# Kernel optimization log

Hardware: AMD Instinct MI355X
Metric: run time of the kernel (lower is better)

## Reference

```python
import jax, jax.numpy as jnp
import numpy as np
import math

B, S, D = 4, 2048, 1024
H, DK, DV = 16, 64, 64
EPS = 1e-5
SCALE = math.sqrt(1.0 / D)  # NOTE: original scales by 1/sqrt(d_model), not 1/sqrt(d_k)


def setup_inputs() -> dict:
    key = jax.random.key(0)
    ks = jax.random.split(key, 12)
    s = 0.02
    return {
        "Q": jax.random.normal(ks[0], (B, S, D), jnp.float32),
        "K": jax.random.normal(ks[1], (B, S, D), jnp.float32),
        "V": jax.random.normal(ks[2], (B, S, D), jnp.float32),
        # stacked per-head projection weights (torch Linear: y = x @ W.T + b)
        "Wq": jax.random.normal(ks[3], (H, D, DK), jnp.float32) * s,
        "bq": jnp.zeros((H, DK), jnp.float32),
        "Wk": jax.random.normal(ks[4], (H, D, DK), jnp.float32) * s,
        "bk": jnp.zeros((H, DK), jnp.float32),
        "Wv": jax.random.normal(ks[5], (H, D, DV), jnp.float32) * s,
        "bv": jnp.zeros((H, DV), jnp.float32),
        "Wo": jax.random.normal(ks[6], (H * DV, D), jnp.float32) * s,
        "bo": jnp.zeros((D,), jnp.float32),
        "gamma": jnp.ones((D,), jnp.float32),
        "beta": jnp.zeros((D,), jnp.float32),
    }


def reference(Q, K, V, Wq, bq, Wk, bk, Wv, bv, Wo, bo, gamma, beta):
    residual = Q
    # batched per-head projections: [B,S,D] x [H,D,dk] -> [B,H,S,dk]
    q = jnp.einsum("bsd,hdk->bhsk", Q, Wq) + bq[None, :, None, :]
    k = jnp.einsum("bsd,hdk->bhsk", K, Wk) + bk[None, :, None, :]
    v = jnp.einsum("bsd,hdv->bhsv", V, Wv) + bv[None, :, None, :]
    # scaled dot-product attention (scale uses d_model, per original code)
    attn = jax.nn.softmax(jnp.einsum("bhsk,bhtk->bhst", q, k) * SCALE, axis=-1)
    out = jnp.einsum("bhst,bhtv->bhsv", attn, v)  # [B,H,S,DV]
    # concat heads along feature dim: [B,S,H*DV]
    out = out.transpose(0, 2, 1, 3).reshape(B, S, H * DV)
    out = out @ Wo + bo  # output projection
    # dropout is identity in eval mode
    out = out + residual
    # BatchNorm1d over (B,S) per channel (training-mode batch stats)
    mean = jnp.mean(out, axis=(0, 1))
    var = jnp.mean(jnp.square(out - mean), axis=(0, 1))
    out = (out - mean) * jax.lax.rsqrt(var + EPS) * gamma + beta
    return out.transpose(0, 2, 1)  # (B, d_model, S)
```

## Files before the change

### kernel.cpp

```cpp
#include <hip/hip_runtime.h>

#define B_ 4
#define S_ 2048
#define D_ 1024
#define H_ 16
#define SCALE_ 0.03125f
#define EPS_ 1e-5f
#define NBS_ 8192

typedef unsigned short ushort_t;
typedef __attribute__((ext_vector_type(8))) short short8;
typedef __attribute__((ext_vector_type(4))) short short4v;
typedef __attribute__((ext_vector_type(4))) float floatx4;
typedef __attribute__((ext_vector_type(2))) unsigned int uint2v;

__device__ __forceinline__ ushort_t f2bf(float f) {
  union { float f; unsigned u; } v; v.f = f;
  unsigned r = v.u + 0x7fffu + ((v.u >> 16) & 1u);
  return (ushort_t)(r >> 16);
}

__device__ __forceinline__ float fast_exp2(float x) {
#if __has_builtin(__builtin_amdgcn_exp2f)
  return __builtin_amdgcn_exp2f(x);
#else
  return __expf(x * 0.6931471805599453f);
#endif
}

__device__ __forceinline__ short8 cvt8(float4 a, float4 b) {
  short8 r;
  r[0] = (short)f2bf(a.x); r[1] = (short)f2bf(a.y);
  r[2] = (short)f2bf(a.z); r[3] = (short)f2bf(a.w);
  r[4] = (short)f2bf(b.x); r[5] = (short)f2bf(b.y);
  r[6] = (short)f2bf(b.z); r[7] = (short)f2bf(b.w);
  return r;
}

__device__ __forceinline__ void gload16(const void* g, void* l) {
  __builtin_amdgcn_global_load_lds(
      (const __attribute__((address_space(1))) unsigned int*)g,
      (__attribute__((address_space(3))) unsigned int*)l, 16, 0, 0);
}

__global__ __launch_bounds__(256) void cvtx_k(const float* __restrict__ src,
                                              ushort_t* __restrict__ dst)
{
  size_t i = ((size_t)blockIdx.x * 256 + threadIdx.x) * 8;
  float4 a = *(const float4*)(src + i);
  float4 b = *(const float4*)(src + i + 4);
  *(short8*)(dst + i) = cvt8(a, b);
}

__global__ __launch_bounds__(256) void wtr_k(const float* __restrict__ src,
                                             ushort_t* __restrict__ dst, int mode)
{
  __shared__ float t[64][65];
  const int tr = blockIdx.x, tc = blockIdx.y;
  const float* sb; int sld;
  if (mode == 0) { sb = src + (size_t)tr * 65536 + (size_t)tc * 64 * 64; sld = 64; }
  else           { sb = src + (size_t)tc * 64 * 1024 + (size_t)tr * 64;  sld = 1024; }
  const int tid = threadIdx.x;
  const int rr = tid >> 2, cs = (tid & 3) * 16;
  const float* p = sb + (size_t)rr * sld + cs;
#pragma unroll
  for (int j = 0; j < 16; ++j) t[rr][cs + j] = p[j];
  __syncthreads();
  ushort_t* dp = dst + (size_t)(tr * 64 + rr) * 1024 + tc * 64 + cs;
#pragma unroll
  for (int j = 0; j < 16; ++j) dp[j] = f2bf(t[cs + j][rr]);
}

__global__ __launch_bounds__(256) void gemm_proj(
    const ushort_t* __restrict__ A, const ushort_t* __restrict__ Bw,
    const float* __restrict__ bias, ushort_t* __restrict__ outp, float scale)
{
  __shared__ ushort_t As[128 * 32];
  __shared__ ushort_t Bs[128 * 32];
  const int tid = threadIdx.x;
  const int wv = tid >> 6, lane = tid & 63, quad = lane >> 4, l16 = lane & 15;
  const int m0 = blockIdx.x * 128, n0 = blockIdx.y * 128;
  const int wm = wv & 1, wn = wv >> 1;
  const int lrow = lane >> 2, lkc = (lane & 3) * 8;

  floatx4 acc[4][4];
#pragma unroll
  for (int i = 0; i < 4; ++i)
#pragma unroll
    for (int j = 0; j < 4; ++j) acc[i][j] = (floatx4){0.f, 0.f, 0.f, 0.f};

  for (int k0 = 0; k0 < 1024; k0 += 32) {
    __syncthreads();
#pragma unroll
    for (int j = 0; j < 2; ++j) {
      const int rb = wv * 32 + j * 16;
      gload16(A + (size_t)(m0 + rb + lrow) * 1024 + k0 + lkc, (char*)As + rb * 64);
      gload16(Bw + (size_t)(n0 + rb + lrow) * 1024 + k0 + lkc, (char*)Bs + rb * 64);
    }
    __syncthreads();
    short8 af[4], bf[4];
#pragma unroll
    for (int i = 0; i < 4; ++i)
      af[i] = *(const short8*)&As[(wm * 64 + i * 16 + l16) * 32 + quad * 8];
#pragma unroll
    for (int i = 0; i < 4; ++i)
      bf[i] = *(const short8*)&Bs[(wn * 64 + i * 16 + l16) * 32 + quad * 8];
#pragma unroll
    for (int mi = 0; mi < 4; ++mi)
#pragma unroll
      for (int ni = 0; ni < 4; ++ni)
        acc[mi][ni] = __builtin_amdgcn_mfma_f32_16x16x32_bf16(
            af[mi], bf[ni], acc[mi][ni], 0, 0, 0);
  }

  const int b = m0 >> 11;
  const int sbase = (m0 & 2047) + wm * 64;
#pragma unroll
  for (int ni = 0; ni < 4; ++ni) {
    const int c = n0 + wn * 64 + ni * 16 + l16;
    const int h = c >> 6, nn = c & 63;
    const float bs = bias[c];
    ushort_t* op = outp + (size_t)(b * 16 + h) * 2048 * 64 + nn;
#pragma unroll
    for (int mi = 0; mi < 4; ++mi)
#pragma unroll
      for (int r = 0; r < 4; ++r) {
        int s = sbase + mi * 16 + quad * 4 + r;
        op[(size_t)s * 64] = f2bf((acc[mi][ni][r] + bs) * scale);
      }
  }
}

__global__ __launch_bounds__(256) void gemm_projT(
    const ushort_t* __restrict__ A, const ushort_t* __restrict__ Bw,
    const float* __restrict__ bias, ushort_t* __restrict__ outp)
{
  __shared__ ushort_t As[128 * 32];
  __shared__ ushort_t Bs[128 * 32];
  const int tid = threadIdx.x;
  const int wv = tid >> 6, lane = tid & 63, quad = lane >> 4, l16 = lane & 15;
  const int m0 = blockIdx.x * 128, n0 = blockIdx.y * 128;
  const int wm = wv & 1, wn = wv >> 1;
  const int lrow = lane >> 2, lkc = (lane & 3) * 8;

  floatx4 acc[4][4];
#pragma unroll
  for (int i = 0; i < 4; ++i)
#pragma unroll
    for (int j = 0; j < 4; ++j) acc[i][j] = (floatx4){0.f, 0.f, 0.f, 0.f};

  for (int k0 = 0; k0 < 1024; k0 += 32) {
    __syncthreads();
#pragma unroll
    for (int j = 0; j < 2; ++j) {
      const int rb = wv * 32 + j * 16;
      gload16(A + (size_t)(m0 + rb + lrow) * 1024 + k0 + lkc, (char*)As + rb * 64);
      gload16(Bw + (size_t)(n0 + rb + lrow) * 1024 + k0 + lkc, (char*)Bs + rb * 64);
    }
    __syncthreads();
    short8 af[4], bf[4];
#pragma unroll
    for (int i = 0; i < 4; ++i)
      af[i] = *(const short8*)&As[(wm * 64 + i * 16 + l16) * 32 + quad * 8];
#pragma unroll
    for (int i = 0; i < 4; ++i)
      bf[i] = *(const short8*)&Bs[(wn * 64 + i * 16 + l16) * 32 + quad * 8];
#pragma unroll
    for (int mi = 0; mi < 4; ++mi)
#pragma unroll
      for (int ni = 0; ni < 4; ++ni)
        acc[mi][ni] = __builtin_amdgcn_mfma_f32_16x16x32_bf16(
            af[mi], bf[ni], acc[mi][ni], 0, 0, 0);
  }

  const int b = m0 >> 11;
  const int sbase = (m0 & 2047) + wm * 64;
#pragma unroll
  for (int ni = 0; ni < 4; ++ni) {
    const int c = n0 + wn * 64 + ni * 16 + l16;
    const int h = c >> 6, nn = c & 63;
    const float bs = bias[c];
    ushort_t* op = outp + ((size_t)(b * 16 + h) * 64 + nn) * 2048;
#pragma unroll
    for (int mi = 0; mi < 4; ++mi) {
      int s0v = sbase + mi * 16 + quad * 4;
      short4v p;
#pragma unroll
      for (int r = 0; r < 4; ++r) p[r] = (short)f2bf(acc[mi][ni][r] + bs);
      *(short4v*)(op + s0v) = p;
    }
  }
}

__global__ __launch_bounds__(256) void gemm_oproj(
    const ushort_t* __restrict__ A, const ushort_t* __restrict__ Bw,
    const float* __restrict__ bo, const float* __restrict__ resid,
    float* __restrict__ y)
{
  __shared__ ushort_t As[128 * 32];
  __shared__ ushort_t Bs[128 * 32];
  const int tid = threadIdx.x;
  const int wv = tid >> 6, lane = tid & 63, quad = lane >> 4, l16 = lane & 15;
  const int m0 = blockIdx.x * 128, n0 = blockIdx.y * 128;
  const int wm = wv & 1, wn = wv >> 1;
  const int lrow = lane >> 2, lkc = (lane & 3) * 8;

  floatx4 acc[4][4];
#pragma unroll
  for (int i = 0; i < 4; ++i)
#pragma unroll
    for (int j = 0; j < 4; ++j) acc[i][j] = (floatx4){0.f, 0.f, 0.f, 0.f};

  for (int k0 = 0; k0 < 1024; k0 += 32) {
    __syncthreads();
#pragma unroll
    for (int j = 0; j < 2; ++j) {
      const int rb = wv * 32 + j * 16;
      gload16(A + (size_t)(m0 + rb + lrow) * 1024 + k0 + lkc, (char*)As + rb * 64);
      gload16(Bw + (size_t)(n0 + rb + lrow) * 1024 + k0 + lkc, (char*)Bs + rb * 64);
    }
    __syncthreads();
    short8 af[4], bf[4];
#pragma unroll
    for (int i = 0; i < 4; ++i)
      af[i] = *(const short8*)&As[(wm * 64 + i * 16 + l16) * 32 + quad * 8];
#pragma unroll
    for (int i = 0; i < 4; ++i)
      bf[i] = *(const short8*)&Bs[(wn * 64 + i * 16 + l16) * 32 + quad * 8];
#pragma unroll
    for (int mi = 0; mi < 4; ++mi)
#pragma unroll
      for (int ni = 0; ni < 4; ++ni)
        acc[mi][ni] = __builtin_amdgcn_mfma_f32_16x16x32_bf16(
            af[mi], bf[ni], acc[mi][ni], 0, 0, 0);
  }

  const int mb = m0 + wm * 64;
#pragma unroll
  for (int ni = 0; ni < 4; ++ni) {
    const int d = n0 + wn * 64 + ni * 16 + l16;
    const float bs = bo[d];
#pragma unroll
    for (int mi = 0; mi < 4; ++mi)
#pragma unroll
      for (int r = 0; r < 4; ++r) {
        int m = mb + mi * 16 + quad * 4 + r;
        y[(size_t)m * 1024 + d] = acc[mi][ni][r] + bs + resid[(size_t)m * 1024 + d];
      }
  }
}

__global__ __launch_bounds__(256, 3) void attn_k(
    const ushort_t* __restrict__ q, const ushort_t* __restrict__ k,
    const ushort_t* __restrict__ vt, ushort_t* __restrict__ ao)
{
  __shared__ ushort_t lds[24576];
  char* ldsb = (char*)lds;
  const int tid = threadIdx.x;
  const int wv = tid >> 6, lane = tid & 63, quad = lane >> 4, l16 = lane & 15;
  const int q0 = blockIdx.x * 128, h = blockIdx.y, b = blockIdx.z;
  const size_t bh = (size_t)(b * H_ + h) * S_;
  const ushort_t* vb = vt + (size_t)(b * H_ + h) * 64 * S_;

  short8 aq[2][2];
#pragma unroll
  for (int rb = 0; rb < 2; ++rb) {
    const ushort_t* qrow = q + (bh + q0 + wv * 32 + rb * 16 + l16) * 64;
    aq[rb][0] = *(const short8*)(qrow + quad * 8);
    aq[rb][1] = *(const short8*)(qrow + 32 + quad * 8);
  }

  floatx4 o[2][4];
  float ll[2] = {0.f, 0.f};
#pragma unroll
  for (int rb = 0; rb < 2; ++rb)
#pragma unroll
    for (int cb = 0; cb < 4; ++cb) o[rb][cb] = (floatx4){0.f, 0.f, 0.f, 0.f};

  const int swz = (l16 & 7) << 4;
  const int q8 = quad * 8;
  const int pb = 32768 + wv * 4096 + l16 * 128;

  auto stage = [&](int nb, int t0) {
#pragma unroll
    for (int i = 0; i < 4; ++i) {
      const int idx = wv * 4 + i;
      const int cb = (idx >> 1) & 3, hf = idx & 1;
      if (idx < 8)
        gload16(k + (bh + t0 + cb * 16 + l16) * 64 + hf * 32 + quad * 8,
                (char*)lds + nb * 8192 + idx * 1024);
      else
        gload16(vb + (size_t)(cb * 16 + l16) * S_ + t0 + hf * 32 + quad * 8,
                (char*)lds + 16384 + nb * 8192 + (idx - 8) * 1024);
    }
  };

  stage(0, 0);
  asm volatile("s_waitcnt vmcnt(0)" ::: "memory");
  __syncthreads();

  for (int t0 = 0; t0 < S_; t0 += 64) {
    const int nb = (t0 >> 6) & 1;
    const ushort_t* KsC = lds + nb * 4096;
    const ushort_t* VsC = lds + 8192 + nb * 4096;
    if (t0 + 64 < S_) stage(nb ^ 1, t0 + 64);

    floatx4 sc[2][4];
#pragma unroll
    for (int rb = 0; rb < 2; ++rb)
#pragma unroll
      for (int cb = 0; cb < 4; ++cb) sc[rb][cb] = (floatx4){0.f, 0.f, 0.f, 0.f};
    __builtin_amdgcn_s_setprio(1);
#pragma unroll
    for (int hf = 0; hf < 2; ++hf) {
      short8 bk[4];
#pragma unroll
      for (int cb = 0; cb < 4; ++cb)
        bk[cb] = *(const short8*)&KsC[(cb * 2 + hf) * 512 + lane * 8];
#pragma unroll
      for (int rb = 0; rb < 2; ++rb)
#pragma unroll
        for (int cb = 0; cb < 4; ++cb)
          sc[rb][cb] = __builtin_amdgcn_mfma_f32_16x16x32_bf16(
              bk[cb], aq[rb][hf], sc[rb][cb], 0, 0, 0);
    }
    __builtin_amdgcn_s_setprio(0);

    short8 bvf[2][4];
#pragma unroll
    for (int hf = 0; hf < 2; ++hf)
#pragma unroll
      for (int cb = 0; cb < 4; ++cb)
        bvf[hf][cb] = *(const short8*)&VsC[(cb * 2 + hf) * 512 + lane * 8];

#pragma unroll
    for (int rb = 0; rb < 2; ++rb) {
#pragma unroll
      for (int cb = 0; cb < 4; ++cb) {
        float p0 = fast_exp2(sc[rb][cb][0]);
        float p1 = fast_exp2(sc[rb][cb][1]);
        float p2 = fast_exp2(sc[rb][cb][2]);
        float p3 = fast_exp2(sc[rb][cb][3]);
        ll[rb] += (p0 + p1) + (p2 + p3);
        uint2v w;
        w[0] = (unsigned)f2bf(p0) | ((unsigned)f2bf(p1) << 16);
        w[1] = (unsigned)f2bf(p2) | ((unsigned)f2bf(p3) << 16);
        *(uint2v*)(ldsb + pb + rb * 2048 + ((cb * 32 + q8) ^ swz)) = w;
      }
    }
    asm volatile("s_waitcnt lgkmcnt(0)" ::: "memory");
    __builtin_amdgcn_sched_barrier(0);

    __builtin_amdgcn_s_setprio(1);
#pragma unroll
    for (int rb = 0; rb < 2; ++rb)
#pragma unroll
      for (int hf = 0; hf < 2; ++hf) {
        short8 ap = *(const short8*)(ldsb + pb + rb * 2048 +
                                     ((hf * 64 + quad * 16) ^ swz));
#pragma unroll
        for (int cb = 0; cb < 4; ++cb)
          o[rb][cb] = __builtin_amdgcn_mfma_f32_16x16x32_bf16(
              ap, bvf[hf][cb], o[rb][cb], 0, 0, 0);
      }
    __builtin_amdgcn_s_setprio(0);

    asm volatile("s_waitcnt vmcnt(0)" ::: "memory");
    __syncthreads();
  }

#pragma unroll
  for (int rb = 0; rb < 2; ++rb) {
    ll[rb] += __shfl_xor(ll[rb], 16);
    ll[rb] += __shfl_xor(ll[rb], 32);
  }
  float linv[2][4];
#pragma unroll
  for (int rb = 0; rb < 2; ++rb)
#pragma unroll
    for (int r = 0; r < 4; ++r)
      linv[rb][r] = 1.f / __shfl(ll[rb], quad * 4 + r);
#pragma unroll
  for (int rb = 0; rb < 2; ++rb)
#pragma unroll
    for (int cb = 0; cb < 4; ++cb)
#pragma unroll
      for (int r = 0; r < 4; ++r) {
        float val = o[rb][cb][r] * linv[rb][r];
        size_t idx = (size_t)(b * S_ + q0 + wv * 32 + rb * 16 + quad * 4 + r) * 1024
                     + h * 64 + cb * 16 + l16;
        ao[idx] = f2bf(val);
      }
}

__global__ __launch_bounds__(256) void stats_k(
    const float* __restrict__ y, float* __restrict__ s1, float* __restrict__ s2)
{
  const int tid = threadIdx.x;
  const int r0 = blockIdx.x * 32;
  float a[4] = {0.f, 0.f, 0.f, 0.f}, bb[4] = {0.f, 0.f, 0.f, 0.f};
  for (int r = 0; r < 32; ++r) {
    const float* row = y + (size_t)(r0 + r) * D_;
#pragma unroll
    for (int j = 0; j < 4; ++j) {
      float vv = row[tid + j * 256];
      a[j] += vv;
      bb[j] += vv * vv;
    }
  }
#pragma unroll
  for (int j = 0; j < 4; ++j) {
    atomicAdd(&s1[tid + j * 256], a[j]);
    atomicAdd(&s2[tid + j * 256], bb[j]);
  }
}

__global__ __launch_bounds__(256) void norm_k(
    const float* __restrict__ y, const float* __restrict__ s1,
    const float* __restrict__ s2, const float* __restrict__ gamma,
    const float* __restrict__ beta, float* __restrict__ out)
{
  __shared__ float tile[64][65];
  __shared__ float scl[64], sft[64];
  const int tid = threadIdx.x;
  const int s0 = blockIdx.x * 64, d0 = blockIdx.y * 64, b = blockIdx.z;

  if (tid < 64) {
    int d = d0 + tid;
    float mean = s1[d] * (1.f / (float)NBS_);
    float var = s2[d] * (1.f / (float)NBS_) - mean * mean;
    float rstd = rsqrtf(var + EPS_);
    float g = gamma[d];
    scl[tid] = rstd * g;
    sft[tid] = beta[d] - mean * rstd * g;
  }
  __syncthreads();

  const int si = tid >> 2, dc = (tid & 3) * 16;
  const float* row = y + (size_t)(b * S_ + s0 + si) * D_ + d0 + dc;
#pragma unroll
  for (int j = 0; j < 16; ++j)
    tile[si][dc + j] = row[j] * scl[dc + j] + sft[dc + j];
  __syncthreads();

  const int di = tid >> 2, sg = (tid & 3) * 16;
  float* dst = out + (size_t)(b * D_ + d0 + di) * S_ + s0 + sg;
#pragma unroll
  for (int jj = 0; jj < 4; ++jj) {
    float4 p;
    p.x = tile[sg + jj * 4 + 0][di];
    p.y = tile[sg + jj * 4 + 1][di];
    p.z = tile[sg + jj * 4 + 2][di];
    p.w = tile[sg + jj * 4 + 3][di];
    *(float4*)(dst + jj * 4) = p;
  }
}

extern "C" void kernel_launch(void* const* d_in, const int* in_sizes, int n_in,
                              void* d_out, int out_size, void* d_ws, size_t ws_size,
                              hipStream_t stream)
{
  (void)in_sizes; (void)n_in; (void)out_size; (void)ws_size;
  const float* Q     = (const float*)d_in[0];
  const float* Kin   = (const float*)d_in[1];
  const float* Vin   = (const float*)d_in[2];
  const float* Wq    = (const float*)d_in[3];
  const float* bq    = (const float*)d_in[4];
  const float* Wk    = (const float*)d_in[5];
  const float* bk    = (const float*)d_in[6];
  const float* Wv    = (const float*)d_in[7];
  const float* bv    = (const float*)d_in[8];
  const float* Wo    = (const float*)d_in[9];
  const float* bo    = (const float*)d_in[10];
  const float* gamma = (const float*)d_in[11];
  const float* beta  = (const float*)d_in[12];
  float* out = (float*)d_out;

  char* ws = (char*)d_ws;
  const size_t MB = 1u << 20;
  ushort_t* xb  = (ushort_t*)(ws);
  ushort_t* wtq = (ushort_t*)(ws + 16 * MB);
  ushort_t* wtk = (ushort_t*)(ws + 18 * MB);
  ushort_t* wtv = (ushort_t*)(ws + 20 * MB);
  ushort_t* wto = (ushort_t*)(ws + 22 * MB);
  ushort_t* qb  = (ushort_t*)(ws + 24 * MB);
  ushort_t* kb  = (ushort_t*)(ws + 40 * MB);
  ushort_t* vtb = (ushort_t*)(ws + 56 * MB);
  ushort_t* ao  = (ushort_t*)(ws);
  float*    y   = (float*)(ws + 24 * MB);
  float*    s1  = (float*)(ws + 56 * MB);
  float*    s2  = (float*)(ws + 56 * MB + 4096);

  wtr_k<<<dim3(16, 16), 256, 0, stream>>>(Wq, wtq, 0);
  wtr_k<<<dim3(16, 16), 256, 0, stream>>>(Wk, wtk, 0);
  wtr_k<<<dim3(16, 16), 256, 0, stream>>>(Wv, wtv, 0);
  wtr_k<<<dim3(16, 16), 256, 0, stream>>>(Wo, wto, 1);

  const float QSC = SCALE_ * 1.44269504088896f;
  cvtx_k<<<4096, 256, 0, stream>>>(Q, xb);
  gemm_proj<<<dim3(64, 8), 256, 0, stream>>>(xb, wtq, bq, qb, QSC);
  cvtx_k<<<4096, 256, 0, stream>>>(Kin, xb);
  gemm_proj<<<dim3(64, 8), 256, 0, stream>>>(xb, wtk, bk, kb, 1.0f);
  cvtx_k<<<4096, 256, 0, stream>>>(Vin, xb);
  gemm_projT<<<dim3(64, 8), 256, 0, stream>>>(xb, wtv, bv, vtb);

  attn_k<<<dim3(16, 16, 4), 256, 0, stream>>>(qb, kb, vtb, ao);
  gemm_oproj<<<dim3(64, 8), 256, 0, stream>>>(ao, wto, bo, Q, y);

  hipMemsetAsync(ws + 56 * MB, 0, 8192, stream);
  stats_k<<<256, 256, 0, stream>>>(y, s1, s2);
  norm_k<<<dim3(32, 16, 4), 256, 0, stream>>>(y, s1, s2, gamma, beta, out);
}
```

Before: 409.9 us.

## Compute softmax row sums via MFMA with ones and use packed bf16 convert

The attention kernel drops the per-lane VALU accumulation of exp values and the final shuffle reduction. It instead computes row sums with an extra MFMA that multiplies the bf16 P tile by a vector of ones. The manual bf16 rounding is replaced with the hardware v_cvt_pk_bf16_f32 instruction. The LDS swizzle is changed to include bit 3, so the P fragment is now read as two 4-element halves. The goal is to take VALU work off the softmax inner loop, at the cost of extra MFMA issue and split LDS reads. Row sums are now taken from bf16-rounded probabilities, which keeps them consistent with the values fed to the PV product.

Result: faster. 400.6 us (-2.3%).

```diff
diff --git a/kernel.cpp b/kernel.cpp
--- a/kernel.cpp
+++ b/kernel.cpp
@@ -28,6 +28,12 @@
 #endif
 }
 
+__device__ __forceinline__ unsigned cvt_pk_bf16(float a, float b) {
+  unsigned r;
+  asm("v_cvt_pk_bf16_f32 %0, %1, %2" : "=v"(r) : "v"(a), "v"(b));
+  return r;
+}
+
 __device__ __forceinline__ short8 cvt8(float4 a, float4 b) {
   short8 r;
   r[0] = (short)f2bf(a.x); r[1] = (short)f2bf(a.y);
@@ -270,14 +276,20 @@
     aq[rb][1] = *(const short8*)(qrow + 32 + quad * 8);
   }
 
+  short8 ones;
+#pragma unroll
+  for (int j = 0; j < 8; ++j) ones[j] = (short)0x3F80;
+
   floatx4 o[2][4];
-  float ll[2] = {0.f, 0.f};
-#pragma unroll
-  for (int rb = 0; rb < 2; ++rb)
+  floatx4 accl[2];
+#pragma unroll
+  for (int rb = 0; rb < 2; ++rb) {
 #pragma unroll
     for (int cb = 0; cb < 4; ++cb) o[rb][cb] = (floatx4){0.f, 0.f, 0.f, 0.f};
-
-  const int swz = (l16 & 7) << 4;
+    accl[rb] = (floatx4){0.f, 0.f, 0.f, 0.f};
+  }
+
+  const int swz = ((l16 & 7) << 4) | (l16 & 8);
   const int q8 = quad * 8;
   const int pb = 32768 + wv * 4096 + l16 * 128;
 
@@ -334,20 +346,18 @@
         bvf[hf][cb] = *(const short8*)&VsC[(cb * 2 + hf) * 512 + lane * 8];
 
 #pragma unroll
-    for (int rb = 0; rb < 2; ++rb) {
+    for (int rb = 0; rb < 2; ++rb)
 #pragma unroll
       for (int cb = 0; cb < 4; ++cb) {
         float p0 = fast_exp2(sc[rb][cb][0]);
         float p1 = fast_exp2(sc[rb][cb][1]);
         float p2 = fast_exp2(sc[rb][cb][2]);
         float p3 = fast_exp2(sc[rb][cb][3]);
-        ll[rb] += (p0 + p1) + (p2 + p3);
         uint2v w;
-        w[0] = (unsigned)f2bf(p0) | ((unsigned)f2bf(p1) << 16);
-        w[1] = (unsigned)f2bf(p2) | ((unsigned)f2bf(p3) << 16);
+        w[0] = cvt_pk_bf16(p0, p1);
+        w[1] = cvt_pk_bf16(p2, p3);
         *(uint2v*)(ldsb + pb + rb * 2048 + ((cb * 32 + q8) ^ swz)) = w;
       }
-    }
     asm volatile("s_waitcnt lgkmcnt(0)" ::: "memory");
     __builtin_amdgcn_sched_barrier(0);
 
@@ -356,12 +366,19 @@
     for (int rb = 0; rb < 2; ++rb)
 #pragma unroll
       for (int hf = 0; hf < 2; ++hf) {
-        short8 ap = *(const short8*)(ldsb + pb + rb * 2048 +
-                                     ((hf * 64 + quad * 16) ^ swz));
+        const char* pr = ldsb + pb + rb * 2048;
+        const int lo = (hf * 64 + quad * 16) ^ swz;
+        short4v a0 = *(const short4v*)(pr + lo);
+        short4v a1 = *(const short4v*)(pr + (lo ^ 8));
+        short8 ap;
+        ap[0] = a0[0]; ap[1] = a0[1]; ap[2] = a0[2]; ap[3] = a0[3];
+        ap[4] = a1[0]; ap[5] = a1[1]; ap[6] = a1[2]; ap[7] = a1[3];
 #pragma unroll
         for (int cb = 0; cb < 4; ++cb)
           o[rb][cb] = __builtin_amdgcn_mfma_f32_16x16x32_bf16(
               ap, bvf[hf][cb], o[rb][cb], 0, 0, 0);
+        accl[rb] = __builtin_amdgcn_mfma_f32_16x16x32_bf16(
+            ap, ones, accl[rb], 0, 0, 0);
       }
     __builtin_amdgcn_s_setprio(0);
 
@@ -369,17 +386,12 @@
     __syncthreads();
   }
 
-#pragma unroll
-  for (int rb = 0; rb < 2; ++rb) {
-    ll[rb] += __shfl_xor(ll[rb], 16);
-    ll[rb] += __shfl_xor(ll[rb], 32);
-  }
   float linv[2][4];
 #pragma unroll
   for (int rb = 0; rb < 2; ++rb)
 #pragma unroll
     for (int r = 0; r < 4; ++r)
-      linv[rb][r] = 1.f / __shfl(ll[rb], quad * 4 + r);
+      linv[rb][r] = 1.f / accl[rb][r];
 #pragma unroll
   for (int rb = 0; rb < 2; ++rb)
 #pragma unroll
```
